# Kernel tuning notes

Hardware: AMD Instinct MI355X
Metric: run time of the kernel (lower is better)

Reference implementation:

```python
import jax, jax.numpy as jnp
import numpy as np

POOL_H, POOL_W = 7, 7


def _crop_and_resize(fmap, boxes, ph, pw):
    # TF tf.image.crop_and_resize (bilinear) semantics, vectorized over all boxes.
    # fmap: [B, H, W, C]; boxes: [B, N, 4] normalized (y1, x1, y2, x2)
    B, H, W, C = fmap.shape
    dt = fmap.dtype
    y1, x1, y2, x2 = (boxes[..., i] for i in range(4))  # each [B, N]
    iy = jnp.arange(ph, dtype=dt)
    ix = jnp.arange(pw, dtype=dt)
    # in_y = y1*(H-1) + i*(y2-y1)*(H-1)/(ph-1)
    ys = y1[..., None] * (H - 1) + iy * ((y2 - y1) * (H - 1) / (ph - 1))[..., None]  # [B,N,ph]
    xs = x1[..., None] * (W - 1) + ix * ((x2 - x1) * (W - 1) / (pw - 1))[..., None]  # [B,N,pw]
    y0f = jnp.floor(ys)
    x0f = jnp.floor(xs)
    y0 = jnp.clip(y0f.astype(jnp.int32), 0, H - 1)
    y1i = jnp.clip(y0 + 1, 0, H - 1)
    x0 = jnp.clip(x0f.astype(jnp.int32), 0, W - 1)
    x1i = jnp.clip(x0 + 1, 0, W - 1)
    fy = (ys - y0f)[:, :, :, None, None]  # [B,N,ph,1,1]
    fx = (xs - x0f)[:, :, None, :, None]  # [B,N,1,pw,1]

    def gather(fb, yi, xi):  # fb [H,W,C], yi [N,ph], xi [N,pw] -> [N,ph,pw,C]
        return fb[yi[:, :, None], xi[:, None, :]]

    g = jax.vmap(gather)
    tl = g(fmap, y0, x0)
    tr = g(fmap, y0, x1i)
    bl = g(fmap, y1i, x0)
    br = g(fmap, y1i, x1i)
    top = tl + (tr - tl) * fx
    bot = bl + (br - bl) * fx
    return top + (bot - top) * fy  # [B,N,ph,pw,C]


def setup_inputs() -> dict:
    key = jax.random.key(0)
    kb, k2, k3, k4, k5 = jax.random.split(key, 5)
    B, N, C = 2, 1000, 256
    # random well-formed boxes: two corners sorted per axis
    pts = jax.random.uniform(kb, (B, N, 2, 2), dtype=jnp.float32)
    lo = jnp.min(pts, axis=2)  # [B,N,2] -> (y, x) mins
    hi = jnp.max(pts, axis=2)
    boxes = jnp.stack([lo[..., 0], lo[..., 1], hi[..., 0], hi[..., 1]], axis=-1)
    # image_meta per compose_image_meta: image_shape lives at [:, 4:7]
    image_meta = jnp.zeros((B, 14), dtype=jnp.float32)
    image_meta = image_meta.at[:, 4].set(1024.0).at[:, 5].set(1024.0).at[:, 6].set(3.0)
    feat2 = jax.random.normal(k2, (B, 256, 256, C), dtype=jnp.float32)
    feat3 = jax.random.normal(k3, (B, 128, 128, C), dtype=jnp.float32)
    feat4 = jax.random.normal(k4, (B, 64, 64, C), dtype=jnp.float32)
    feat5 = jax.random.normal(k5, (B, 32, 32, C), dtype=jnp.float32)
    return {"boxes": boxes, "image_meta": image_meta, "feat2": feat2,
            "feat3": feat3, "feat4": feat4, "feat5": feat5}


def reference(boxes, image_meta, feat2, feat3, feat4, feat5):
    boxes = jax.lax.stop_gradient(boxes)  # matches tf.stop_gradient on level_boxes
    h = boxes[..., 2] - boxes[..., 0]  # [B,N]
    w = boxes[..., 3] - boxes[..., 1]
    img_shape = image_meta[0, 4:7]
    image_area = img_shape[0] * img_shape[1]
    lvl = jnp.log2(jnp.sqrt(h * w) / (224.0 / jnp.sqrt(image_area)))
    roi_level = jnp.clip(4.0 + jnp.round(lvl), 2.0, 5.0).astype(jnp.int32)  # [B,N]
    out = jnp.zeros(boxes.shape[:2] + (POOL_H, POOL_W, feat2.shape[-1]), dtype=feat2.dtype)
    for i, fm in enumerate((feat2, feat3, feat4, feat5)):
        crop = _crop_and_resize(fm, boxes, POOL_H, POOL_W)
        sel = (roi_level == (i + 2))[:, :, None, None, None]
        out = out + jnp.where(sel, crop, jnp.zeros((), dtype=crop.dtype))
    return out
```

## Files before the change

kernel.cpp:

```cpp
#include <hip/hip_runtime.h>


__global__ __launch_bounds__(64) void roi_align_kernel(
    const float* __restrict__ boxes,
    const float* __restrict__ meta,
    const float* __restrict__ f2,
    const float* __restrict__ f3,
    const float* __restrict__ f4,
    const float* __restrict__ f5,
    float* __restrict__ out,
    int N)
{
    const int C = 256;
    int cell = blockIdx.x;
    int bn   = cell / 49;
    int pc   = cell - bn * 49;
    int py   = pc / 7;
    int px   = pc - py * 7;
    int b    = bn / N;

    float y1 = boxes[bn * 4 + 0];
    float x1 = boxes[bn * 4 + 1];
    float y2 = boxes[bn * 4 + 2];
    float x2 = boxes[bn * 4 + 3];
    float h = y2 - y1;
    float w = x2 - x1;

    float area = meta[4] * meta[5];
    float lvl  = log2f(sqrtf(h * w) / (224.0f / sqrtf(area)));
    float rl   = 4.0f + rintf(lvl);
    rl = fminf(fmaxf(rl, 2.0f), 5.0f);
    int level = (int)rl;

    const float* fm;
    int H;
    if (level == 2)      { fm = f2; H = 256; }
    else if (level == 3) { fm = f3; H = 128; }
    else if (level == 4) { fm = f4; H = 64;  }
    else                 { fm = f5; H = 32;  }
    int W = H;

    float sy = (h * (float)(H - 1)) / 6.0f;
    float sx = (w * (float)(W - 1)) / 6.0f;
    float ys = y1 * (float)(H - 1) + (float)py * sy;
    float xs = x1 * (float)(W - 1) + (float)px * sx;
    float y0f = floorf(ys);
    float x0f = floorf(xs);
    int y0 = min(max((int)y0f, 0), H - 1);
    int yi = min(y0 + 1, H - 1);
    int x0 = min(max((int)x0f, 0), W - 1);
    int xi = min(x0 + 1, W - 1);
    float fy = ys - y0f;
    float fx = xs - x0f;

    size_t base = (size_t)b * H * W * C;
    const float4* ptl = (const float4*)(fm + base + ((size_t)y0 * W + x0) * C);
    const float4* ptr = (const float4*)(fm + base + ((size_t)y0 * W + xi) * C);
    const float4* pbl = (const float4*)(fm + base + ((size_t)yi * W + x0) * C);
    const float4* pbr = (const float4*)(fm + base + ((size_t)yi * W + xi) * C);

    int t = threadIdx.x;
    float4 tl = ptl[t];
    float4 tr = ptr[t];
    float4 bl = pbl[t];
    float4 br = pbr[t];

    float4 o;
    {
        float top = tl.x + (tr.x - tl.x) * fx;
        float bot = bl.x + (br.x - bl.x) * fx;
        o.x = top + (bot - top) * fy;
    }
    {
        float top = tl.y + (tr.y - tl.y) * fx;
        float bot = bl.y + (br.y - bl.y) * fx;
        o.y = top + (bot - top) * fy;
    }
    {
        float top = tl.z + (tr.z - tl.z) * fx;
        float bot = bl.z + (br.z - bl.z) * fx;
        o.z = top + (bot - top) * fy;
    }
    {
        float top = tl.w + (tr.w - tl.w) * fx;
        float bot = bl.w + (br.w - bl.w) * fx;
        o.w = top + (bot - top) * fy;
    }

    float4* po = (float4*)(out + (size_t)cell * C);
    po[t] = o;
}

extern "C" void kernel_launch(void* const* d_in, const int* in_sizes, int n_in,
                              void* d_out, int out_size, void* d_ws, size_t ws_size,
                              hipStream_t stream) {
    const float* boxes = (const float*)d_in[0];
    const float* meta  = (const float*)d_in[1];
    const float* f2    = (const float*)d_in[2];
    const float* f3    = (const float*)d_in[3];
    const float* f4    = (const float*)d_in[4];
    const float* f5    = (const float*)d_in[5];
    float* out = (float*)d_out;

    int B = in_sizes[1] / 14;
    int N = in_sizes[0] / (4 * B);

    int grid = B * N * 49;
    roi_align_kernel<<<grid, 64, 0, stream>>>(boxes, meta, f2, f3, f4, f5, out, N);
}
```

Baseline: 249.3 us.

## Process one box per 256-thread block with waves looping over pooled cells

```diff
diff --git a/kernel.cpp b/kernel.cpp
--- a/kernel.cpp
+++ b/kernel.cpp
@@ -1,7 +1,7 @@
 #include <hip/hip_runtime.h>
 
 
-__global__ __launch_bounds__(64) void roi_align_kernel(
+__global__ __launch_bounds__(256) void roi_align_kernel(
     const float* __restrict__ boxes,
     const float* __restrict__ meta,
     const float* __restrict__ f2,
@@ -12,12 +12,8 @@
     int N)
 {
     const int C = 256;
-    int cell = blockIdx.x;
-    int bn   = cell / 49;
-    int pc   = cell - bn * 49;
-    int py   = pc / 7;
-    int px   = pc - py * 7;
-    int b    = bn / N;
+    int bn = blockIdx.x;
+    int b  = bn / N;
 
     float y1 = boxes[bn * 4 + 0];
     float x1 = boxes[bn * 4 + 1];
@@ -42,53 +38,64 @@
 
     float sy = (h * (float)(H - 1)) / 6.0f;
     float sx = (w * (float)(W - 1)) / 6.0f;
-    float ys = y1 * (float)(H - 1) + (float)py * sy;
-    float xs = x1 * (float)(W - 1) + (float)px * sx;
-    float y0f = floorf(ys);
-    float x0f = floorf(xs);
-    int y0 = min(max((int)y0f, 0), H - 1);
-    int yi = min(y0 + 1, H - 1);
-    int x0 = min(max((int)x0f, 0), W - 1);
-    int xi = min(x0 + 1, W - 1);
-    float fy = ys - y0f;
-    float fx = xs - x0f;
+    float ybase = y1 * (float)(H - 1);
+    float xbase = x1 * (float)(W - 1);
 
-    size_t base = (size_t)b * H * W * C;
-    const float4* ptl = (const float4*)(fm + base + ((size_t)y0 * W + x0) * C);
-    const float4* ptr = (const float4*)(fm + base + ((size_t)y0 * W + xi) * C);
-    const float4* pbl = (const float4*)(fm + base + ((size_t)yi * W + x0) * C);
-    const float4* pbr = (const float4*)(fm + base + ((size_t)yi * W + xi) * C);
+    const float* fb = fm + (size_t)b * H * W * C;
+    float* ob = out + (size_t)bn * 49 * C;
 
-    int t = threadIdx.x;
-    float4 tl = ptl[t];
-    float4 tr = ptr[t];
-    float4 bl = pbl[t];
-    float4 br = pbr[t];
+    int wave = threadIdx.x >> 6;
+    int lane = threadIdx.x & 63;
 
-    float4 o;
-    {
-        float top = tl.x + (tr.x - tl.x) * fx;
-        float bot = bl.x + (br.x - bl.x) * fx;
-        o.x = top + (bot - top) * fy;
+    for (int pc = wave; pc < 49; pc += 4) {
+        int py = pc / 7;
+        int px = pc - py * 7;
+
+        float ys = ybase + (float)py * sy;
+        float xs = xbase + (float)px * sx;
+        float y0f = floorf(ys);
+        float x0f = floorf(xs);
+        int y0 = min(max((int)y0f, 0), H - 1);
+        int yi = min(y0 + 1, H - 1);
+        int x0 = min(max((int)x0f, 0), W - 1);
+        int xi = min(x0 + 1, W - 1);
+        float fy = ys - y0f;
+        float fx = xs - x0f;
+
+        const float4* ptl = (const float4*)(fb + ((size_t)y0 * W + x0) * C);
+        const float4* ptr = (const float4*)(fb + ((size_t)y0 * W + xi) * C);
+        const float4* pbl = (const float4*)(fb + ((size_t)yi * W + x0) * C);
+        const float4* pbr = (const float4*)(fb + ((size_t)yi * W + xi) * C);
+
+        float4 tl = ptl[lane];
+        float4 tr = ptr[lane];
+        float4 bl = pbl[lane];
+        float4 br = pbr[lane];
+
+        float4 o;
+        {
+            float top = tl.x + (tr.x - tl.x) * fx;
+            float bot = bl.x + (br.x - bl.x) * fx;
+            o.x = top + (bot - top) * fy;
+        }
+        {
+            float top = tl.y + (tr.y - tl.y) * fx;
+            float bot = bl.y + (br.y - bl.y) * fx;
+            o.y = top + (bot - top) * fy;
+        }
+        {
+            float top = tl.z + (tr.z - tl.z) * fx;
+            float bot = bl.z + (br.z - bl.z) * fx;
+            o.z = top + (bot - top) * fy;
+        }
+        {
+            float top = tl.w + (tr.w - tl.w) * fx;
+            float bot = bl.w + (br.w - bl.w) * fx;
+            o.w = top + (bot - top) * fy;
+        }
+
+        ((float4*)(ob + (size_t)pc * C))[lane] = o;
     }
-    {
-        float top = tl.y + (tr.y - tl.y) * fx;
-        float bot = bl.y + (br.y - bl.y) * fx;
-        o.y = top + (bot - top) * fy;
-    }
-    {
-        float top = tl.z + (tr.z - tl.z) * fx;
-        float bot = bl.z + (br.z - bl.z) * fx;
-        o.z = top + (bot - top) * fy;
-    }
-    {
-        float top = tl.w + (tr.w - tl.w) * fx;
-        float bot = bl.w + (br.w - bl.w) * fx;
-        o.w = top + (bot - top) * fy;
-    }
-
-    float4* po = (float4*)(out + (size_t)cell * C);
-    po[t] = o;
 }
 
 extern "C" void kernel_launch(void* const* d_in, const int* in_sizes, int n_in,
@@ -105,6 +112,6 @@
     int B = in_sizes[1] / 14;
     int N = in_sizes[0] / (4 * B);
 
-    int grid = B * N * 49;
-    roi_align_kernel<<<grid, 64, 0, stream>>>(boxes, meta, f2, f3, f4, f5, out, N);
+    int grid = B * N;
+    roi_align_kernel<<<grid, 256, 0, stream>>>(boxes, meta, f2, f3, f4, f5, out, N);
 }
```

Measured after the change: 257.3 us. 1.03x slower.
